# Performance work log

Measured on AMD Instinct MI355X. Metric: run time of the kernel, lower is better.

## Reference

```python
import jax, jax.numpy as jnp
import numpy as np

N = 100_000   # nodes per node type (A, B)
H = 128       # hidden_size == input feature dim
E = 600_000   # edges per relation
L = 2         # num_layers
R = 3         # relations: 0:(A->B), 1:(B->B), 2:(B->A)
AA = 64       # attn_size
C = 16        # num_classes
NEG_SLOPE = 0.01
BN_EPS = 1.0


def setup_inputs() -> dict:
    key = jax.random.key(0)
    ks = jax.random.split(key, 24)
    s = 1.0 / np.sqrt(H)
    inp = {
        "xA": jax.random.normal(ks[0], (N, H), jnp.float32),
        "xB": jax.random.normal(ks[1], (N, H), jnp.float32),
        "Wsrc": jax.random.uniform(ks[2], (L, R, H, H), jnp.float32, -s, s),
        "bsrc": jax.random.uniform(ks[3], (L, R, H), jnp.float32, -s, s),
        "Wdst": jax.random.uniform(ks[4], (L, R, H, H), jnp.float32, -s, s),
        "bdst": jax.random.uniform(ks[5], (L, R, H), jnp.float32, -s, s),
        "Wupd": jax.random.uniform(ks[6], (L, R, 2 * H, H), jnp.float32, -s, s),
        "bupd": jax.random.uniform(ks[7], (L, R, H), jnp.float32, -s, s),
        "attnW1": jax.random.uniform(ks[8], (L, H, AA), jnp.float32, -s, s),
        "attnb1": jax.random.uniform(ks[9], (L, AA), jnp.float32, -s, s),
        "attnw2": jax.random.uniform(ks[10], (L, AA), jnp.float32, -s, s),
        "gamma": jnp.ones((L, 2, H), jnp.float32),
        "beta": jnp.zeros((L, 2, H), jnp.float32),
        "fcW": jax.random.uniform(ks[11], (2, H, C), jnp.float32, -s, s),
        "fcb": jax.random.uniform(ks[12], (2, C), jnp.float32, -s, s),
        "eAB": jax.random.randint(ks[13], (2, E), 0, N, jnp.int32),
        "eBB": jax.random.randint(ks[14], (2, E), 0, N, jnp.int32),
        "eBA": jax.random.randint(ks[15], (2, E), 0, N, jnp.int32),
    }
    return inp


def _scatter_mean(src_feat, dst_idx, num_dst):
    # mean-aggregate gathered src features onto dst nodes (SpMM mean)
    seg = jax.ops.segment_sum(src_feat, dst_idx, num_segments=num_dst)
    cnt = jax.ops.segment_sum(
        jnp.ones((dst_idx.shape[0], 1), src_feat.dtype), dst_idx, num_segments=num_dst)
    return seg / jnp.maximum(cnt, 1.0)


def reference(xA, xB, Wsrc, bsrc, Wdst, bdst, Wupd, bupd,
              attnW1, attnb1, attnw2, gamma, beta, fcW, fcb,
              eAB, eBB, eBA):

    def conv(l, r, xs, xd, e):
        aggr = _scatter_mean(xs[e[0]], e[1], xd.shape[0])   # [Nd, H]
        h = jnp.concatenate(
            [xd @ Wdst[l, r] + bdst[l, r], aggr @ Wsrc[l, r] + bsrc[l, r]], axis=-1)
        return h @ Wupd[l, r] + bupd[l, r]

    def attn_combine(xs, l):
        # xs: [K, N, H]; per-relation attention score, softmax over K (detached)
        s = jnp.tanh(xs @ attnW1[l] + attnb1[l]) @ attnw2[l]   # [K, N]
        alpha = jax.lax.stop_gradient(jax.nn.softmax(s.mean(axis=-1)))  # [K]
        return jnp.einsum('k,knh->nh', alpha, xs)

    def bn(x, g, b):
        mu = x.mean(axis=0)
        var = x.var(axis=0)  # biased, as torch BN training forward
        return (x - mu) / jnp.sqrt(var + BN_EPS) * g + b

    def leaky(x):
        return jnp.where(x >= 0, x, NEG_SLOPE * x)

    for l in range(L):
        embB1 = conv(l, 0, xA, xB, eAB)  # A -> B
        embB2 = conv(l, 1, xB, xB, eBB)  # B -> B
        embA = conv(l, 2, xB, xA, eBA)   # B -> A (single relation, no combine)
        xB_new = attn_combine(jnp.stack([embB1, embB2]), l)
        xA = leaky(bn(embA, gamma[l, 0], beta[l, 0]))
        xB = leaky(bn(xB_new, gamma[l, 1], beta[l, 1]))

    outA = xA @ fcW[0] + fcb[0]
    outB = xB @ fcW[1] + fcb[1]
    return jnp.stack([outA, outB])  # [2, N, C]
```

## Files before the change

### kernel.cpp

```cpp
#include <hip/hip_runtime.h>

#define NN 100000
#define HH 128
#define EE 600000
#define LL 2
#define RR 3
#define AAA 64
#define CC 16
#define SCAN_B 98
#define ATTN_GRID ((NN + 127) / 128)

typedef unsigned short u16;
typedef unsigned int u32;
typedef __attribute__((ext_vector_type(8))) short bf16x8;
typedef __attribute__((ext_vector_type(4))) float f32x4;

__device__ inline u16 f2bf(float f) {
    unsigned int u = __float_as_uint(f);
    return (u16)((u + 0x7FFF + ((u >> 16) & 1)) >> 16);
}
__device__ inline float bf2f(u16 h) { return __uint_as_float((unsigned int)h << 16); }

__device__ __forceinline__ int hi_off(int gi, int r) { return (gi * 32) ^ ((r & 7) << 4); }
__device__ __forceinline__ int lo_off(int gi, int r) { return (gi * 32 + 16) ^ ((r & 7) << 4); }

__device__ __forceinline__ void stage16(const void* g, void* l) {
    __builtin_amdgcn_global_load_lds((const __attribute__((address_space(1))) unsigned int*)g,
                                     (__attribute__((address_space(3))) unsigned int*)l, 16, 0, 0);
}

__global__ void k_fuse_w(const float* __restrict__ Wsrc, const float* __restrict__ Wdst,
                         const float* __restrict__ Wupd, u16* __restrict__ Wdt_hi,
                         u16* __restrict__ Wdt_lo, u16* __restrict__ Wst_hi,
                         u16* __restrict__ Wst_lo) {
    int b = blockIdx.x;
    int lr = b >> 7, i = b & 127;
    int t = threadIdx.x;
    int j = t & 127;
    const float* wu = Wupd + (size_t)lr * 2 * HH * HH;
    float acc = 0.f;
    size_t o = ((size_t)lr * HH + j) * HH + i;
    if (t < 128) {
        const float* wd = Wdst + ((size_t)lr * HH + i) * HH;
        for (int k = 0; k < HH; ++k) acc += wd[k] * wu[k * HH + j];
        u16 h = f2bf(acc);
        Wdt_hi[o] = h;
        Wdt_lo[o] = f2bf(acc - bf2f(h));
    } else {
        const float* wsc = Wsrc + ((size_t)lr * HH + i) * HH;
        for (int k = 0; k < HH; ++k) acc += wsc[k] * wu[(HH + k) * HH + j];
        u16 h = f2bf(acc);
        Wst_hi[o] = h;
        Wst_lo[o] = f2bf(acc - bf2f(h));
    }
}

__global__ void k_fuse_b(const float* __restrict__ bsrc, const float* __restrict__ bdst,
                         const float* __restrict__ bupd, const float* __restrict__ Wupd,
                         float* __restrict__ fB) {
    int lr = blockIdx.x;
    int j = threadIdx.x;
    const float* wu = Wupd + (size_t)lr * 2 * HH * HH;
    const float* bd = bdst + lr * HH;
    const float* bs = bsrc + lr * HH;
    float acc = bupd[lr * HH + j];
    for (int k = 0; k < HH; ++k)
        acc += bd[k] * wu[k * HH + j] + bs[k] * wu[(HH + k) * HH + j];
    fB[lr * HH + j] = acc;
}

__global__ void k_fuse_a(const float* __restrict__ W1, u16* __restrict__ Ah,
                         u16* __restrict__ Al) {
    int b = blockIdx.x;
    int l = b >> 6, a = b & 63;
    int k = threadIdx.x;
    float v = W1[((size_t)l * HH + k) * AAA + a];
    u16 h = f2bf(v);
    size_t o = (size_t)b * HH + k;
    Ah[o] = h;
    Al[o] = f2bf(v - bf2f(h));
}

__global__ void k_count(const int* __restrict__ e0, const int* __restrict__ e1,
                        const int* __restrict__ e2, int* __restrict__ cnt,
                        int* __restrict__ pose) {
    int rel = blockIdx.y;
    const int* d = (rel == 0 ? e0 : rel == 1 ? e1 : e2) + EE;
    int i = blockIdx.x * 256 + threadIdx.x;
    if (i < EE) pose[rel * EE + i] = atomicAdd(&cnt[rel * NN + d[i]], 1);
}

__global__ void k_scan1(const int* __restrict__ cnt_all, int* __restrict__ rs_all,
                        int* __restrict__ bsum) {
    __shared__ int sd[256];
    int rel = blockIdx.y;
    const int* cnt = cnt_all + rel * NN;
    int* rs = rs_all + rel * NN;
    int blk = blockIdx.x, tid = threadIdx.x;
    int base = blk * 1024 + tid * 4;
    int c0 = 0, c1 = 0, c2 = 0, c3 = 0;
    if (base + 0 < NN) c0 = cnt[base + 0];
    if (base + 1 < NN) c1 = cnt[base + 1];
    if (base + 2 < NN) c2 = cnt[base + 2];
    if (base + 3 < NN) c3 = cnt[base + 3];
    int s = c0 + c1 + c2 + c3;
    sd[tid] = s;
    __syncthreads();
    for (int off = 1; off < 256; off <<= 1) {
        int v = (tid >= off) ? sd[tid - off] : 0;
        __syncthreads();
        sd[tid] += v;
        __syncthreads();
    }
    int excl = sd[tid] - s;
    if (tid == 255) bsum[rel * 128 + blk] = sd[255];
    if (base + 0 < NN) rs[base + 0] = excl;
    if (base + 1 < NN) rs[base + 1] = excl + c0;
    if (base + 2 < NN) rs[base + 2] = excl + c0 + c1;
    if (base + 3 < NN) rs[base + 3] = excl + c0 + c1 + c2;
}

__global__ void k_scan2(int* __restrict__ bsum) {
    __shared__ int sd[128];
    int rel = blockIdx.x;
    int tid = threadIdx.x;
    int v = (tid < SCAN_B) ? bsum[rel * 128 + tid] : 0;
    sd[tid] = v;
    __syncthreads();
    for (int off = 1; off < 128; off <<= 1) {
        int u = (tid >= off) ? sd[tid - off] : 0;
        __syncthreads();
        sd[tid] += u;
        __syncthreads();
    }
    if (tid < SCAN_B) bsum[rel * 128 + tid] = sd[tid] - v;
}

__global__ void k_scan3(int* __restrict__ rs_all, const int* __restrict__ bsum) {
    int rel = blockIdx.y;
    int i = blockIdx.x * 256 + threadIdx.x;
    if (i < NN) rs_all[rel * NN + i] += bsum[rel * 128 + (i >> 10)];
}

__global__ void k_fill(const int* __restrict__ e0, const int* __restrict__ e1,
                       const int* __restrict__ e2, const int* __restrict__ pose,
                       const int* __restrict__ rs_all, int* __restrict__ csr_all) {
    int rel = blockIdx.y;
    const int* e = rel == 0 ? e0 : rel == 1 ? e1 : e2;
    int i = blockIdx.x * 256 + threadIdx.x;
    if (i >= EE) return;
    int s = e[i], d = e[EE + i];
    csr_all[(size_t)rel * EE + rs_all[rel * NN + d] + pose[rel * EE + i]] = s;
}

__global__ __launch_bounds__(256) void k_aggr(u16* __restrict__ Xp, const float* __restrict__ xs,
                                              const int* __restrict__ rs, const int* __restrict__ cnt,
                                              const int* __restrict__ csr,
                                              const float* __restrict__ bnsc) {
    int node = blockIdx.x * 4 + (threadIdx.x >> 6);
    if (node >= NN) return;
    int lane = threadIdx.x & 63;
    int beg = rs[node], deg = cnt[node];
    const float2* xs2 = (const float2*)xs;
    bool bn = bnsc != nullptr;
    float2 scv = make_float2(1.f, 1.f), sfv = make_float2(0.f, 0.f);
    if (bn) {
        scv = ((const float2*)bnsc)[lane];
        sfv = ((const float2*)(bnsc + 128))[lane];
    }
    auto xf = [&](float2 v) {
        if (bn) {
            v.x = v.x * scv.x + sfv.x;
            v.y = v.y * scv.y + sfv.y;
            v.x = v.x >= 0.f ? v.x : 0.01f * v.x;
            v.y = v.y >= 0.f ? v.y : 0.01f * v.y;
        }
        return v;
    };
    float ax = 0.f, ay = 0.f;
    int j = 0;
    for (; j + 4 <= deg; j += 4) {
        int s0 = csr[beg + j], s1 = csr[beg + j + 1];
        int s2 = csr[beg + j + 2], s3 = csr[beg + j + 3];
        float2 v0 = xf(xs2[(size_t)s0 * 64 + lane]);
        float2 v1 = xf(xs2[(size_t)s1 * 64 + lane]);
        float2 v2 = xf(xs2[(size_t)s2 * 64 + lane]);
        float2 v3 = xf(xs2[(size_t)s3 * 64 + lane]);
        ax += (v0.x + v1.x) + (v2.x + v3.x);
        ay += (v0.y + v1.y) + (v2.y + v3.y);
    }
    if (j + 2 <= deg) {
        int s0 = csr[beg + j], s1 = csr[beg + j + 1];
        float2 v0 = xf(xs2[(size_t)s0 * 64 + lane]);
        float2 v1 = xf(xs2[(size_t)s1 * 64 + lane]);
        ax += v0.x + v1.x;
        ay += v0.y + v1.y;
        j += 2;
    }
    if (j < deg) {
        float2 v = xf(xs2[(size_t)csr[beg + j] * 64 + lane]);
        ax += v.x;
        ay += v.y;
    }
    float sc = 1.0f / fmaxf((float)deg, 1.0f);
    float vx = ax * sc, vy = ay * sc;
    u16 hx = f2bf(vx), hy = f2bf(vy);
    u16 lx = f2bf(vx - bf2f(hx)), ly = f2bf(vy - bf2f(hy));
    int g = lane >> 2;
    char* base = (char*)Xp + (size_t)node * 512 + (g >> 2) * 128;
    int jb = (lane & 3) * 4;
    __builtin_nontemporal_store(((u32)hy << 16) | hx, (u32*)(base + hi_off(g & 3, node) + jb));
    __builtin_nontemporal_store(((u32)ly << 16) | lx, (u32*)(base + lo_off(g & 3, node) + jb));
}

__global__ __launch_bounds__(256) void k_cgemm(float* Y, const u16* X1p,
                                               const float* __restrict__ X2,
                                               const u16* __restrict__ W1h, const u16* __restrict__ W1l,
                                               const u16* __restrict__ W2h, const u16* __restrict__ W2l,
                                               const float* __restrict__ bias, int nrows,
                                               const float* __restrict__ bnsc2,
                                               float* __restrict__ colsum) {
    __shared__ __attribute__((aligned(16))) char Xt[16384];
    int tid = threadIdx.x;
    int row0 = blockIdx.x * 128;
    int lane = tid & 63, wv = tid >> 6;
    int l15 = lane & 15, lg = lane >> 4;
    bool full = (row0 + 128 <= nrows);

    f32x4 acc[8][2];
#pragma unroll
    for (int i = 0; i < 8; ++i)
#pragma unroll
        for (int j = 0; j < 2; ++j) acc[i][j] = (f32x4)(0.f);

    for (int ph = 0; ph < 2; ++ph) {
        const u16* Wh = ph ? W2h : W1h;
        const u16* Wl = ph ? W2l : W1l;
        for (int kc = 0; kc < HH; kc += 32) {
            __syncthreads();
            if (ph == 0) {
#pragma unroll
                for (int p = 0; p < 4; ++p) {
                    int tb = p * 4096 + tid * 16;
                    int r = tb >> 7, off = tb & 127;
                    stage16((const char*)X1p + (size_t)(row0 + r) * 512 + (kc >> 5) * 128 + off,
                            Xt + tb);
                }
            } else {
#pragma unroll
                for (int it = 0; it < 2; ++it) {
                    int g2 = tid + it * 256;
                    int r = g2 >> 2, gi = g2 & 3;
                    float4 a = make_float4(0.f, 0.f, 0.f, 0.f), b = a;
                    if (full || row0 + r < nrows) {
                        const float* xp = &X2[(size_t)(row0 + r) * HH + kc + gi * 8];
                        a = *(const float4*)xp;
                        b = *(const float4*)(xp + 4);
                    }
                    if (bnsc2) {
                        const float* scp = bnsc2 + kc + gi * 8;
                        const float* sfp = bnsc2 + 128 + kc + gi * 8;
                        float4 s0 = *(const float4*)scp, s1 = *(const float4*)(scp + 4);
                        float4 f0 = *(const float4*)sfp, f1 = *(const float4*)(sfp + 4);
                        a.x = a.x * s0.x + f0.x; a.y = a.y * s0.y + f0.y;
                        a.z = a.z * s0.z + f0.z; a.w = a.w * s0.w + f0.w;
                        b.x = b.x * s1.x + f1.x; b.y = b.y * s1.y + f1.y;
                        b.z = b.z * s1.z + f1.z; b.w = b.w * s1.w + f1.w;
                        a.x = a.x >= 0.f ? a.x : 0.01f * a.x;
                        a.y = a.y >= 0.f ? a.y : 0.01f * a.y;
                        a.z = a.z >= 0.f ? a.z : 0.01f * a.z;
                        a.w = a.w >= 0.f ? a.w : 0.01f * a.w;
                        b.x = b.x >= 0.f ? b.x : 0.01f * b.x;
                        b.y = b.y >= 0.f ? b.y : 0.01f * b.y;
                        b.z = b.z >= 0.f ? b.z : 0.01f * b.z;
                        b.w = b.w >= 0.f ? b.w : 0.01f * b.w;
                    }
                    u16 h0 = f2bf(a.x), h1 = f2bf(a.y), h2 = f2bf(a.z), h3 = f2bf(a.w);
                    u16 h4 = f2bf(b.x), h5 = f2bf(b.y), h6 = f2bf(b.z), h7 = f2bf(b.w);
                    bf16x8 hv = {(short)h0, (short)h1, (short)h2, (short)h3,
                                 (short)h4, (short)h5, (short)h6, (short)h7};
                    bf16x8 lv = {(short)f2bf(a.x - bf2f(h0)), (short)f2bf(a.y - bf2f(h1)),
                                 (short)f2bf(a.z - bf2f(h2)), (short)f2bf(a.w - bf2f(h3)),
                                 (short)f2bf(b.x - bf2f(h4)), (short)f2bf(b.y - bf2f(h5)),
                                 (short)f2bf(b.z - bf2f(h6)), (short)f2bf(b.w - bf2f(h7))};
                    char* rb = Xt + r * 128;
                    *(bf16x8*)(rb + hi_off(gi, r)) = hv;
                    *(bf16x8*)(rb + lo_off(gi, r)) = lv;
                }
            }
            bf16x8 bh[2], bl[2];
#pragma unroll
            for (int nt = 0; nt < 2; ++nt) {
                int n = (wv * 2 + nt) * 16 + l15;
                bh[nt] = *(const bf16x8*)&Wh[(size_t)n * HH + kc + lg * 8];
                bl[nt] = *(const bf16x8*)&Wl[(size_t)n * HH + kc + lg * 8];
            }
            __syncthreads();
#pragma unroll
            for (int mt = 0; mt < 8; ++mt) {
                int r = mt * 16 + l15;
                const char* rb = Xt + r * 128;
                bf16x8 ah = *(const bf16x8*)(rb + hi_off(lg, r));
                bf16x8 al = *(const bf16x8*)(rb + lo_off(lg, r));
#pragma unroll
                for (int nt = 0; nt < 2; ++nt) {
                    acc[mt][nt] = __builtin_amdgcn_mfma_f32_16x16x32_bf16(ah, bh[nt], acc[mt][nt], 0, 0, 0);
                    acc[mt][nt] = __builtin_amdgcn_mfma_f32_16x16x32_bf16(ah, bl[nt], acc[mt][nt], 0, 0, 0);
                    acc[mt][nt] = __builtin_amdgcn_mfma_f32_16x16x32_bf16(al, bh[nt], acc[mt][nt], 0, 0, 0);
                }
            }
        }
    }
#pragma unroll
    for (int nt = 0; nt < 2; ++nt) {
        int ncol = (wv * 2 + nt) * 16 + l15;
        float bv = bias[ncol];
        float s = 0.f, q = 0.f;
#pragma unroll
        for (int mt = 0; mt < 8; ++mt)
#pragma unroll
            for (int j = 0; j < 4; ++j) {
                int r = row0 + mt * 16 + lg * 4 + j;
                if (r < nrows) {
                    float y = acc[mt][nt][j] + bv;
                    Y[(size_t)r * HH + ncol] = y;
                    s += y;
                    q += y * y;
                }
            }
        if (colsum) {
            s += __shfl_xor(s, 16); s += __shfl_xor(s, 32);
            q += __shfl_xor(q, 16); q += __shfl_xor(q, 32);
            if (lg == 0) {
                atomicAdd(&colsum[ncol], s);
                atomicAdd(&colsum[128 + ncol], q);
            }
        }
    }
}

__global__ __launch_bounds__(256) void k_attn(const float* __restrict__ XA, const float* __restrict__ XB,
                                              const u16* __restrict__ Ah, const u16* __restrict__ Al,
                                              const float* __restrict__ b1, const float* __restrict__ w2,
                                              float* __restrict__ PA, float* __restrict__ PB, int nrows) {
    __shared__ __attribute__((aligned(16))) char Xt[16384];
    __shared__ float red[4];
    int tid = threadIdx.x;
    bool second = blockIdx.x >= ATTN_GRID;
    const float* X = second ? XB : XA;
    float* partial = second ? PB : PA;
    int row0 = (second ? blockIdx.x - ATTN_GRID : blockIdx.x) * 128;
    int lane = tid & 63, wv = tid >> 6;
    int l15 = lane & 15, lg = lane >> 4;
    bool full = (row0 + 128 <= nrows);

    f32x4 acc[8];
#pragma unroll
    for (int i = 0; i < 8; ++i) acc[i] = (f32x4)(0.f);

    for (int kc = 0; kc < HH; kc += 32) {
        __syncthreads();
#pragma unroll
        for (int it = 0; it < 2; ++it) {
            int g2 = tid + it * 256;
            int r = g2 >> 2, gi = g2 & 3;
            float4 a = make_float4(0.f, 0.f, 0.f, 0.f), b = a;
            if (full || row0 + r < nrows) {
                const float* xp = &X[(size_t)(row0 + r) * HH + kc + gi * 8];
                a = *(const float4*)xp;
                b = *(const float4*)(xp + 4);
            }
            u16 h0 = f2bf(a.x), h1 = f2bf(a.y), h2 = f2bf(a.z), h3 = f2bf(a.w);
            u16 h4 = f2bf(b.x), h5 = f2bf(b.y), h6 = f2bf(b.z), h7 = f2bf(b.w);
            bf16x8 hv = {(short)h0, (short)h1, (short)h2, (short)h3,
                         (short)h4, (short)h5, (short)h6, (short)h7};
            bf16x8 lv = {(short)f2bf(a.x - bf2f(h0)), (short)f2bf(a.y - bf2f(h1)),
                         (short)f2bf(a.z - bf2f(h2)), (short)f2bf(a.w - bf2f(h3)),
                         (short)f2bf(b.x - bf2f(h4)), (short)f2bf(b.y - bf2f(h5)),
                         (short)f2bf(b.z - bf2f(h6)), (short)f2bf(b.w - bf2f(h7))};
            char* rb = Xt + r * 128;
            *(bf16x8*)(rb + hi_off(gi, r)) = hv;
            *(bf16x8*)(rb + lo_off(gi, r)) = lv;
        }
        int a = wv * 16 + l15;
        bf16x8 bh = *(const bf16x8*)&Ah[(size_t)a * HH + kc + lg * 8];
        bf16x8 bl = *(const bf16x8*)&Al[(size_t)a * HH + kc + lg * 8];
        __syncthreads();
#pragma unroll
        for (int mt = 0; mt < 8; ++mt) {
            int r = mt * 16 + l15;
            const char* rb = Xt + r * 128;
            bf16x8 ah = *(const bf16x8*)(rb + hi_off(lg, r));
            bf16x8 al = *(const bf16x8*)(rb + lo_off(lg, r));
            acc[mt] = __builtin_amdgcn_mfma_f32_16x16x32_bf16(ah, bh, acc[mt], 0, 0, 0);
            acc[mt] = __builtin_amdgcn_mfma_f32_16x16x32_bf16(ah, bl, acc[mt], 0, 0, 0);
            acc[mt] = __builtin_amdgcn_mfma_f32_16x16x32_bf16(al, bh, acc[mt], 0, 0, 0);
        }
    }
    float b1v = b1[wv * 16 + l15];
    float w2v = w2[wv * 16 + l15];
    float tot = 0.f;
#pragma unroll
    for (int mt = 0; mt < 8; ++mt)
#pragma unroll
        for (int j = 0; j < 4; ++j) {
            int r = row0 + mt * 16 + lg * 4 + j;
            if (r < nrows) tot += tanhf(acc[mt][j] + b1v) * w2v;
        }
#pragma unroll
    for (int off = 32; off > 0; off >>= 1) tot += __shfl_xor(tot, off);
    if (lane == 0) red[wv] = tot;
    __syncthreads();
    if (tid == 0)
        partial[second ? (blockIdx.x - ATTN_GRID) : blockIdx.x] = red[0] + red[1] + red[2] + red[3];
}

__global__ void k_alpha(const float* __restrict__ P1, const float* __restrict__ P2,
                        float* __restrict__ alpha, int nparts, float invn) {
    __shared__ float s1[256], s2[256];
    int tid = threadIdx.x;
    float a = 0.f, b = 0.f;
    for (int i = tid; i < nparts; i += 256) { a += P1[i]; b += P2[i]; }
    s1[tid] = a; s2[tid] = b;
    __syncthreads();
    for (int off = 128; off > 0; off >>= 1) {
        if (tid < off) { s1[tid] += s1[tid + off]; s2[tid] += s2[tid + off]; }
        __syncthreads();
    }
    if (tid == 0) {
        float m1 = s1[0] * invn, m2 = s2[0] * invn;
        float mx = fmaxf(m1, m2);
        float e1 = expf(m1 - mx), e2 = expf(m2 - mx);
        float inv = 1.f / (e1 + e2);
        alpha[0] = e1 * inv; alpha[1] = e2 * inv;
    }
}

__global__ __launch_bounds__(256) void k_comb(float* __restrict__ X, const float* __restrict__ Y,
                                              const float* __restrict__ alpha, float* __restrict__ colsum,
                                              float* __restrict__ colsq, int nrows) {
    int tid = threadIdx.x;
    int h = tid & 127, half = tid >> 7;
    float a0 = alpha[0], a1 = alpha[1];
    float s = 0.f, q = 0.f;
    for (int n = blockIdx.x * 2 + half; n < nrows; n += gridDim.x * 2) {
        size_t off = (size_t)n * HH + h;
        float v = a0 * X[off] + a1 * Y[off];
        X[off] = v;
        s += v; q += v * v;
    }
    __shared__ float ls[256], lq[256];
    ls[tid] = s; lq[tid] = q;
    __syncthreads();
    if (half == 0) {
        atomicAdd(&colsum[h], ls[tid] + ls[tid + 128]);
        atomicAdd(&colsq[h], lq[tid] + lq[tid + 128]);
    }
}

__global__ void k_bnp(const float* __restrict__ sum, const float* __restrict__ sq,
                      const float* __restrict__ gamma, const float* __restrict__ beta,
                      float* __restrict__ scale, float* __restrict__ shift, float invn) {
    int h = threadIdx.x;
    float mu = sum[h] * invn;
    float var = sq[h] * invn - mu * mu;
    float sc = gamma[h] * rsqrtf(var + 1.0f);
    scale[h] = sc;
    shift[h] = beta[h] - mu * sc;
}

__global__ __launch_bounds__(256) void k_fc(const float* __restrict__ X0, const float* __restrict__ X1,
                                            const float* __restrict__ sc0, const float* __restrict__ sc1,
                                            const float* __restrict__ Wall, const float* __restrict__ ball,
                                            float* __restrict__ out, int nrows) {
    __shared__ float Xl[64 * 132];
    __shared__ float Wl[HH * CC];
    __shared__ float bl[CC];
    __shared__ float scl[HH], sfl[HH];
    int which = blockIdx.y;
    const float* X = which ? X1 : X0;
    const float* scp = which ? sc1 : sc0;
    const float* W = Wall + which * HH * CC;
    float* o = out + (size_t)which * NN * CC;
    int tid = threadIdx.x;
    int row0 = blockIdx.x * 64;
    for (int i = tid * 4; i < HH * CC; i += 1024)
        *(float4*)&Wl[i] = *(const float4*)&W[i];
    if (tid < CC) bl[tid] = ball[which * CC + tid];
    if (tid < HH) { scl[tid] = scp[tid]; sfl[tid] = scp[128 + tid]; }
    __syncthreads();
    for (int idx = tid; idx < 2048; idx += 256) {
        int r = idx >> 5, cc = idx & 31;
        int n = row0 + r;
        float4 v = make_float4(0.f, 0.f, 0.f, 0.f);
        if (n < nrows) v = *(const float4*)&X[(size_t)n * HH + cc * 4];
        float4 sc = *(const float4*)&scl[cc * 4];
        float4 sf = *(const float4*)&sfl[cc * 4];
        v.x = v.x * sc.x + sf.x; v.y = v.y * sc.y + sf.y;
        v.z = v.z * sc.z + sf.z; v.w = v.w * sc.w + sf.w;
        v.x = v.x >= 0.f ? v.x : 0.01f * v.x;
        v.y = v.y >= 0.f ? v.y : 0.01f * v.y;
        v.z = v.z >= 0.f ? v.z : 0.01f * v.z;
        v.w = v.w >= 0.f ? v.w : 0.01f * v.w;
        *(float4*)&Xl[r * 132 + cc * 4] = v;
    }
    __syncthreads();
    int c = tid & 15, nl = tid >> 4;
    const float* x0 = &Xl[(nl + 0) * 132];
    const float* x1 = &Xl[(nl + 16) * 132];
    const float* x2 = &Xl[(nl + 32) * 132];
    const float* x3 = &Xl[(nl + 48) * 132];
    float a0 = bl[c], a1 = a0, a2 = a0, a3 = a0;
#pragma unroll 8
    for (int h = 0; h < HH; ++h) {
        float w = Wl[h * CC + c];
        a0 += x0[h] * w;
        a1 += x1[h] * w;
        a2 += x2[h] * w;
        a3 += x3[h] * w;
    }
    int n0 = row0 + nl;
    if (n0 < nrows) o[(size_t)n0 * CC + c] = a0;
    if (n0 + 16 < nrows) o[(size_t)(n0 + 16) * CC + c] = a1;
    if (n0 + 32 < nrows) o[(size_t)(n0 + 32) * CC + c] = a2;
    if (n0 + 48 < nrows) o[(size_t)(n0 + 48) * CC + c] = a3;
}

extern "C" void kernel_launch(void* const* d_in, const int* in_sizes, int n_in,
                              void* d_out, int out_size, void* d_ws, size_t ws_size,
                              hipStream_t stream) {
    const float* xA = (const float*)d_in[0];
    const float* xB = (const float*)d_in[1];
    const float* Wsrc = (const float*)d_in[2];
    const float* bsrc = (const float*)d_in[3];
    const float* Wdst = (const float*)d_in[4];
    const float* bdst = (const float*)d_in[5];
    const float* Wupd = (const float*)d_in[6];
    const float* bupd = (const float*)d_in[7];
    const float* attnW1 = (const float*)d_in[8];
    const float* attnb1 = (const float*)d_in[9];
    const float* attnw2 = (const float*)d_in[10];
    const float* gamma = (const float*)d_in[11];
    const float* beta = (const float*)d_in[12];
    const float* fcW = (const float*)d_in[13];
    const float* fcb = (const float*)d_in[14];
    const int* eAB = (const int*)d_in[15];
    const int* eBB = (const int*)d_in[16];
    const int* eBA = (const int*)d_in[17];
    float* out = (float*)d_out;

    float* ws = (float*)d_ws;
    const size_t NH = (size_t)NN * HH;
    const size_t LRHH = (size_t)LL * RR * HH * HH;
    const size_t LAH = (size_t)LL * AAA * HH;
    float* B0 = ws;
    float* B1 = B0 + NH;
    float* B2 = B1 + NH;
    float* B3 = B2 + NH;
    u16* uWdh = (u16*)(B3 + NH);
    u16* uWdl = uWdh + LRHH;
    u16* uWsh = uWdl + LRHH;
    u16* uWsl = uWsh + LRHH;
    u16* uA1h = uWsl + LRHH;
    u16* uA1l = uA1h + LAH;
    float* fB = (float*)(uA1l + LAH);
    float* csA = fB + LL * RR * HH;
    float* csB = csA + 256;
    float* scA = csB + 256;
    float* scB = scA + 256;
    float* scA2 = scB + 256;
    float* scB2 = scA2 + 256;
    float* P1 = scB2 + 256;
    float* P2 = P1 + 1024;
    float* alp = P2 + 1024;
    int* icnt = (int*)(alp + 64);
    int* irs = icnt + 3 * NN;
    int* icsr = irs + 3 * NN;
    int* ifill = icsr + 3 * EE;
    int* ibsum = ifill + 3 * NN;
    int* pose = (int*)B3;
    const float invN = 1.0f / (float)NN;

    k_fuse_w<<<LL * RR * HH, 256, 0, stream>>>(Wsrc, Wdst, Wupd, uWdh, uWdl, uWsh, uWsl);
    k_fuse_b<<<LL * RR, HH, 0, stream>>>(bsrc, bdst, bupd, Wupd, fB);
    k_fuse_a<<<LL * AAA, HH, 0, stream>>>(attnW1, uA1h, uA1l);

    hipMemsetAsync(icnt, 0, 3 * NN * 4, stream);
    k_count<<<dim3((EE + 255) / 256, 3), 256, 0, stream>>>(eAB, eBB, eBA, icnt, pose);
    k_scan1<<<dim3(SCAN_B, 3), 256, 0, stream>>>(icnt, irs, ibsum);
    k_scan2<<<3, 128, 0, stream>>>(ibsum);
    k_scan3<<<dim3((NN + 255) / 256, 3), 256, 0, stream>>>(irs, ibsum);
    k_fill<<<dim3((EE + 255) / 256, 3), 256, 0, stream>>>(eAB, eBB, eBA, pose, irs, icsr);

    const int GEMM_GRID = (NN + 127) / 128;
    const int AGGR_GRID = (NN + 3) / 4;

    auto conv = [&](float* dest, const float* xs, const float* xd, int rel, int lr,
                    const float* bn_xs, const float* bn_xd, float* stats) {
        k_aggr<<<AGGR_GRID, 256, 0, stream>>>((u16*)dest, xs, irs + rel * NN, icnt + rel * NN,
                                              icsr + (size_t)rel * EE, bn_xs);
        k_cgemm<<<GEMM_GRID, 256, 0, stream>>>(dest, (const u16*)dest, xd,
                                               uWsh + (size_t)lr * HH * HH, uWsl + (size_t)lr * HH * HH,
                                               uWdh + (size_t)lr * HH * HH, uWdl + (size_t)lr * HH * HH,
                                               fB + lr * HH, NN, bn_xd, stats);
    };

    hipMemsetAsync(csA, 0, 512 * 4, stream);
    conv(B0, xA, xB, 0, 0, nullptr, nullptr, nullptr);
    conv(B1, xB, xB, 1, 1, nullptr, nullptr, nullptr);
    conv(B2, xB, xA, 2, 2, nullptr, nullptr, csA);
    k_attn<<<2 * ATTN_GRID, 256, 0, stream>>>(B0, B1, uA1h, uA1l, attnb1, attnw2, P1, P2, NN);
    k_alpha<<<1, 256, 0, stream>>>(P1, P2, alp, ATTN_GRID, invN);
    k_comb<<<512, 256, 0, stream>>>(B0, B1, alp, csB, csB + 128, NN);
    k_bnp<<<1, 128, 0, stream>>>(csA, csA + 128, gamma + 0 * HH, beta + 0 * HH, scA, scA + 128, invN);
    k_bnp<<<1, 128, 0, stream>>>(csB, csB + 128, gamma + 1 * HH, beta + 1 * HH, scB, scB + 128, invN);

    hipMemsetAsync(csA, 0, 512 * 4, stream);
    conv(B1, B2, B0, 0, 3, scA, scB, nullptr);
    conv(B3, B0, B0, 1, 4, scB, scB, nullptr);
    k_attn<<<2 * ATTN_GRID, 256, 0, stream>>>(B1, B3, uA1h + (size_t)AAA * HH,
                                              uA1l + (size_t)AAA * HH,
                                              attnb1 + AAA, attnw2 + AAA, P1, P2, NN);
    k_alpha<<<1, 256, 0, stream>>>(P1, P2, alp, ATTN_GRID, invN);
    k_comb<<<512, 256, 0, stream>>>(B1, B3, alp, csB, csB + 128, NN);
    conv(B3, B0, B2, 2, 5, scB, scA, csA);
    k_bnp<<<1, 128, 0, stream>>>(csA, csA + 128, gamma + 2 * HH, beta + 2 * HH, scA2, scA2 + 128, invN);
    k_bnp<<<1, 128, 0, stream>>>(csB, csB + 128, gamma + 3 * HH, beta + 3 * HH, scB2, scB2 + 128, invN);

    k_fc<<<dim3((NN + 63) / 64, 2), 256, 0, stream>>>(B3, B1, scA2, scB2, fcW, fcb, out, NN);
}
```

Before: 1.057 ms.

## Double-buffer LDS staging in GEMM and attention kernels to overlap loads with MFMA

Both the combined GEMM and the attention-score kernel now use two 16 KB shared-memory tiles and stage the next K-chunk while MFMAs consume the current one, cutting from two barriers per chunk to one. This aims to hide global-load and bf16-split conversion latency behind matrix work. It doubles LDS use per block, which may lower occupancy, and adds register pressure from unrolling the whole chunk loop.

```diff
diff --git a/kernel.cpp b/kernel.cpp
--- a/kernel.cpp
+++ b/kernel.cpp
@@ -220,7 +220,7 @@
                                                const float* __restrict__ bias, int nrows,
                                                const float* __restrict__ bnsc2,
                                                float* __restrict__ colsum) {
-    __shared__ __attribute__((aligned(16))) char Xt[16384];
+    __shared__ __attribute__((aligned(16))) char Xt[2][16384];
     int tid = threadIdx.x;
     int row0 = blockIdx.x * 128;
     int lane = tid & 63, wv = tid >> 6;
@@ -233,81 +233,88 @@
 #pragma unroll
         for (int j = 0; j < 2; ++j) acc[i][j] = (f32x4)(0.f);
 
-    for (int ph = 0; ph < 2; ++ph) {
-        const u16* Wh = ph ? W2h : W1h;
-        const u16* Wl = ph ? W2l : W1l;
-        for (int kc = 0; kc < HH; kc += 32) {
-            __syncthreads();
-            if (ph == 0) {
-#pragma unroll
-                for (int p = 0; p < 4; ++p) {
-                    int tb = p * 4096 + tid * 16;
-                    int r = tb >> 7, off = tb & 127;
-                    stage16((const char*)X1p + (size_t)(row0 + r) * 512 + (kc >> 5) * 128 + off,
-                            Xt + tb);
+    auto stage_chunk = [&](int c) {
+        char* dst = Xt[c & 1];
+        if (c < 4) {
+#pragma unroll
+            for (int p = 0; p < 4; ++p) {
+                int tb = p * 4096 + tid * 16;
+                int r = tb >> 7, off = tb & 127;
+                stage16((const char*)X1p + (size_t)(row0 + r) * 512 + (c & 3) * 128 + off,
+                        dst + tb);
+            }
+        } else {
+            int kc = (c & 3) * 32;
+#pragma unroll
+            for (int it = 0; it < 2; ++it) {
+                int g2 = tid + it * 256;
+                int r = g2 >> 2, gi = g2 & 3;
+                float4 a = make_float4(0.f, 0.f, 0.f, 0.f), b = a;
+                if (full || row0 + r < nrows) {
+                    const float* xp = &X2[(size_t)(row0 + r) * HH + kc + gi * 8];
+                    a = *(const float4*)xp;
+                    b = *(const float4*)(xp + 4);
                 }
-            } else {
-#pragma unroll
-                for (int it = 0; it < 2; ++it) {
-                    int g2 = tid + it * 256;
-                    int r = g2 >> 2, gi = g2 & 3;
-                    float4 a = make_float4(0.f, 0.f, 0.f, 0.f), b = a;
-                    if (full || row0 + r < nrows) {
-                        const float* xp = &X2[(size_t)(row0 + r) * HH + kc + gi * 8];
-                        a = *(const float4*)xp;
-                        b = *(const float4*)(xp + 4);
-                    }
-                    if (bnsc2) {
-                        const float* scp = bnsc2 + kc + gi * 8;
-                        const float* sfp = bnsc2 + 128 + kc + gi * 8;
-                        float4 s0 = *(const float4*)scp, s1 = *(const float4*)(scp + 4);
-                        float4 f0 = *(const float4*)sfp, f1 = *(const float4*)(sfp + 4);
-                        a.x = a.x * s0.x + f0.x; a.y = a.y * s0.y + f0.y;
-                        a.z = a.z * s0.z + f0.z; a.w = a.w * s0.w + f0.w;
-                        b.x = b.x * s1.x + f1.x; b.y = b.y * s1.y + f1.y;
-                        b.z = b.z * s1.z + f1.z; b.w = b.w * s1.w + f1.w;
-                        a.x = a.x >= 0.f ? a.x : 0.01f * a.x;
-                        a.y = a.y >= 0.f ? a.y : 0.01f * a.y;
-                        a.z = a.z >= 0.f ? a.z : 0.01f * a.z;
-                        a.w = a.w >= 0.f ? a.w : 0.01f * a.w;
-                        b.x = b.x >= 0.f ? b.x : 0.01f * b.x;
-                        b.y = b.y >= 0.f ? b.y : 0.01f * b.y;
-                        b.z = b.z >= 0.f ? b.z : 0.01f * b.z;
-                        b.w = b.w >= 0.f ? b.w : 0.01f * b.w;
-                    }
-                    u16 h0 = f2bf(a.x), h1 = f2bf(a.y), h2 = f2bf(a.z), h3 = f2bf(a.w);
-                    u16 h4 = f2bf(b.x), h5 = f2bf(b.y), h6 = f2bf(b.z), h7 = f2bf(b.w);
-                    bf16x8 hv = {(short)h0, (short)h1, (short)h2, (short)h3,
-                                 (short)h4, (short)h5, (short)h6, (short)h7};
-                    bf16x8 lv = {(short)f2bf(a.x - bf2f(h0)), (short)f2bf(a.y - bf2f(h1)),
-                                 (short)f2bf(a.z - bf2f(h2)), (short)f2bf(a.w - bf2f(h3)),
-                                 (short)f2bf(b.x - bf2f(h4)), (short)f2bf(b.y - bf2f(h5)),
-                                 (short)f2bf(b.z - bf2f(h6)), (short)f2bf(b.w - bf2f(h7))};
-                    char* rb = Xt + r * 128;
-                    *(bf16x8*)(rb + hi_off(gi, r)) = hv;
-                    *(bf16x8*)(rb + lo_off(gi, r)) = lv;
+                if (bnsc2) {
+                    const float* scp = bnsc2 + kc + gi * 8;
+                    const float* sfp = bnsc2 + 128 + kc + gi * 8;
+                    float4 s0 = *(const float4*)scp, s1 = *(const float4*)(scp + 4);
+                    float4 f0 = *(const float4*)sfp, f1 = *(const float4*)(sfp + 4);
+                    a.x = a.x * s0.x + f0.x; a.y = a.y * s0.y + f0.y;
+                    a.z = a.z * s0.z + f0.z; a.w = a.w * s0.w + f0.w;
+                    b.x = b.x * s1.x + f1.x; b.y = b.y * s1.y + f1.y;
+                    b.z = b.z * s1.z + f1.z; b.w = b.w * s1.w + f1.w;
+                    a.x = a.x >= 0.f ? a.x : 0.01f * a.x;
+                    a.y = a.y >= 0.f ? a.y : 0.01f * a.y;
+                    a.z = a.z >= 0.f ? a.z : 0.01f * a.z;
+                    a.w = a.w >= 0.f ? a.w : 0.01f * a.w;
+                    b.x = b.x >= 0.f ? b.x : 0.01f * b.x;
+                    b.y = b.y >= 0.f ? b.y : 0.01f * b.y;
+                    b.z = b.z >= 0.f ? b.z : 0.01f * b.z;
+                    b.w = b.w >= 0.f ? b.w : 0.01f * b.w;
                 }
+                u16 h0 = f2bf(a.x), h1 = f2bf(a.y), h2 = f2bf(a.z), h3 = f2bf(a.w);
+                u16 h4 = f2bf(b.x), h5 = f2bf(b.y), h6 = f2bf(b.z), h7 = f2bf(b.w);
+                bf16x8 hv = {(short)h0, (short)h1, (short)h2, (short)h3,
+                             (short)h4, (short)h5, (short)h6, (short)h7};
+                bf16x8 lv = {(short)f2bf(a.x - bf2f(h0)), (short)f2bf(a.y - bf2f(h1)),
+                             (short)f2bf(a.z - bf2f(h2)), (short)f2bf(a.w - bf2f(h3)),
+                             (short)f2bf(b.x - bf2f(h4)), (short)f2bf(b.y - bf2f(h5)),
+                             (short)f2bf(b.z - bf2f(h6)), (short)f2bf(b.w - bf2f(h7))};
+                char* rb = dst + r * 128;
+                *(bf16x8*)(rb + hi_off(gi, r)) = hv;
+                *(bf16x8*)(rb + lo_off(gi, r)) = lv;
             }
-            bf16x8 bh[2], bl[2];
+        }
+    };
+
+    stage_chunk(0);
+#pragma unroll
+    for (int c = 0; c < 8; ++c) {
+        const u16* Wh = (c < 4) ? W1h : W2h;
+        const u16* Wl = (c < 4) ? W1l : W2l;
+        int kc = (c & 3) * 32;
+        bf16x8 bh[2], bl[2];
+#pragma unroll
+        for (int nt = 0; nt < 2; ++nt) {
+            int n = (wv * 2 + nt) * 16 + l15;
+            bh[nt] = *(const bf16x8*)&Wh[(size_t)n * HH + kc + lg * 8];
+            bl[nt] = *(const bf16x8*)&Wl[(size_t)n * HH + kc + lg * 8];
+        }
+        __syncthreads();
+        if (c < 7) stage_chunk(c + 1);
+        const char* buf = Xt[c & 1];
+#pragma unroll
+        for (int mt = 0; mt < 8; ++mt) {
+            int r = mt * 16 + l15;
+            const char* rb = buf + r * 128;
+            bf16x8 ah = *(const bf16x8*)(rb + hi_off(lg, r));
+            bf16x8 al = *(const bf16x8*)(rb + lo_off(lg, r));
 #pragma unroll
             for (int nt = 0; nt < 2; ++nt) {
-                int n = (wv * 2 + nt) * 16 + l15;
-                bh[nt] = *(const bf16x8*)&Wh[(size_t)n * HH + kc + lg * 8];
-                bl[nt] = *(const bf16x8*)&Wl[(size_t)n * HH + kc + lg * 8];
-            }
-            __syncthreads();
-#pragma unroll
-            for (int mt = 0; mt < 8; ++mt) {
-                int r = mt * 16 + l15;
-                const char* rb = Xt + r * 128;
-                bf16x8 ah = *(const bf16x8*)(rb + hi_off(lg, r));
-                bf16x8 al = *(const bf16x8*)(rb + lo_off(lg, r));
-#pragma unroll
-                for (int nt = 0; nt < 2; ++nt) {
-                    acc[mt][nt] = __builtin_amdgcn_mfma_f32_16x16x32_bf16(ah, bh[nt], acc[mt][nt], 0, 0, 0);
-                    acc[mt][nt] = __builtin_amdgcn_mfma_f32_16x16x32_bf16(ah, bl[nt], acc[mt][nt], 0, 0, 0);
-                    acc[mt][nt] = __builtin_amdgcn_mfma_f32_16x16x32_bf16(al, bh[nt], acc[mt][nt], 0, 0, 0);
-                }
+                acc[mt][nt] = __builtin_amdgcn_mfma_f32_16x16x32_bf16(ah, bh[nt], acc[mt][nt], 0, 0, 0);
+                acc[mt][nt] = __builtin_amdgcn_mfma_f32_16x16x32_bf16(ah, bl[nt], acc[mt][nt], 0, 0, 0);
+                acc[mt][nt] = __builtin_amdgcn_mfma_f32_16x16x32_bf16(al, bh[nt], acc[mt][nt], 0, 0, 0);
             }
         }
     }
@@ -343,7 +350,7 @@
                                               const u16* __restrict__ Ah, const u16* __restrict__ Al,
                                               const float* __restrict__ b1, const float* __restrict__ w2,
                                               float* __restrict__ PA, float* __restrict__ PB, int nrows) {
-    __shared__ __attribute__((aligned(16))) char Xt[16384];
+    __shared__ __attribute__((aligned(16))) char Xt[2][16384];
     __shared__ float red[4];
     int tid = threadIdx.x;
     bool second = blockIdx.x >= ATTN_GRID;
@@ -358,8 +365,9 @@
 #pragma unroll
     for (int i = 0; i < 8; ++i) acc[i] = (f32x4)(0.f);
 
-    for (int kc = 0; kc < HH; kc += 32) {
-        __syncthreads();
+    auto stage_chunk = [&](int c) {
+        char* dst = Xt[c & 1];
+        int kc = c * 32;
 #pragma unroll
         for (int it = 0; it < 2; ++it) {
             int g2 = tid + it * 256;
@@ -378,18 +386,26 @@
                          (short)f2bf(a.z - bf2f(h2)), (short)f2bf(a.w - bf2f(h3)),
                          (short)f2bf(b.x - bf2f(h4)), (short)f2bf(b.y - bf2f(h5)),
                          (short)f2bf(b.z - bf2f(h6)), (short)f2bf(b.w - bf2f(h7))};
-            char* rb = Xt + r * 128;
+            char* rb = dst + r * 128;
             *(bf16x8*)(rb + hi_off(gi, r)) = hv;
             *(bf16x8*)(rb + lo_off(gi, r)) = lv;
         }
+    };
+
+    stage_chunk(0);
+#pragma unroll
+    for (int c = 0; c < 4; ++c) {
+        int kc = c * 32;
         int a = wv * 16 + l15;
         bf16x8 bh = *(const bf16x8*)&Ah[(size_t)a * HH + kc + lg * 8];
         bf16x8 bl = *(const bf16x8*)&Al[(size_t)a * HH + kc + lg * 8];
         __syncthreads();
+        if (c < 3) stage_chunk(c + 1);
+        const char* buf = Xt[c & 1];
 #pragma unroll
         for (int mt = 0; mt < 8; ++mt) {
             int r = mt * 16 + l15;
-            const char* rb = Xt + r * 128;
+            const char* rb = buf + r * 128;
             bf16x8 ah = *(const bf16x8*)(rb + hi_off(lg, r));
             bf16x8 al = *(const bf16x8*)(rb + lo_off(lg, r));
             acc[mt] = __builtin_amdgcn_mfma_f32_16x16x32_bf16(ah, bh, acc[mt], 0, 0, 0);
```

New measurement: 1.025 ms. -3.0%, faster.
